# Kernel optimization log

Hardware: AMD Instinct MI355X
Metric: run time of the kernel (lower is better)

## Reference

```python
import jax, jax.numpy as jnp
import numpy as np

NUM_NODES = 100000
NUM_EDGES = 1600000
EMBED_DIM = 128
NUM_CLASSES = 2
NUM_LAYERS = 3


def setup_inputs() -> dict:
    key = jax.random.key(0)
    k_row, k_col, k_val, k_emb, k_a, k_w, k_b = jax.random.split(key, 7)
    node_indices = jnp.arange(NUM_NODES, dtype=jnp.int64 if jax.config.read('jax_enable_x64') else jnp.int32)
    adj_row = jax.random.randint(k_row, (NUM_EDGES,), 0, NUM_NODES)
    adj_col = jax.random.randint(k_col, (NUM_EDGES,), 0, NUM_NODES)
    # symmetric-normalized-ish positive edge weights
    adj_val = jax.random.uniform(k_val, (NUM_EDGES,), dtype=jnp.float32) * (1.0 / 16.0)
    embedding = jax.random.normal(k_emb, (NUM_NODES, EMBED_DIM), dtype=jnp.float32)
    alpha = jnp.ones((NUM_LAYERS + 1,), dtype=jnp.float32) / (NUM_LAYERS + 1)
    W = jax.random.normal(k_w, (EMBED_DIM, NUM_CLASSES), dtype=jnp.float32) * 0.05
    b = jnp.zeros((NUM_CLASSES,), dtype=jnp.float32)
    return {
        'node_indices': node_indices, 'adj_row': adj_row, 'adj_col': adj_col,
        'adj_val': adj_val, 'embedding': embedding, 'alpha': alpha, 'W': W, 'b': b,
    }


def reference(node_indices, adj_row, adj_col, adj_val, embedding, alpha, W, b):
    # x: [N, D] embedding lookup
    x = embedding[node_indices]
    a = jax.nn.softmax(alpha)
    # alpha-weighted running sum over propagation layers (dropout in eval mode = identity)
    acc = a[0] * x
    cur = x
    for i in range(NUM_LAYERS):
        # sparse SpMM: out[r] += val * cur[c] for each edge (r, c)
        msgs = adj_val[:, None] * cur[adj_col]          # [E, D]
        cur = jax.ops.segment_sum(msgs, adj_row, num_segments=NUM_NODES)
        acc = acc + a[i + 1] * cur
    return acc @ W + b  # [N, num_classes]
```

## Files before the change

### kernel.cpp

```cpp
#include <hip/hip_runtime.h>

#define GD(x,y) (((x)+(y)-1)/(y))

#define SH   10
#define BPR  (1 << SH)
#define G1   256
#define BS   256
#define KSPL 8

__global__ void histb_k(const int* __restrict__ row, int* __restrict__ cnt,
                        int E, int NBK, int chunk){
    __shared__ int h[128];
    for (int i = threadIdx.x; i < NBK; i += BS) h[i] = 0;
    __syncthreads();
    int s = blockIdx.x * chunk, e = min(E, s + chunk);
    for (int i = s + threadIdx.x; i < e; i += BS)
        atomicAdd(&h[row[i] >> SH], 1);
    __syncthreads();
    for (int i = threadIdx.x; i < NBK; i += BS)
        cnt[(size_t)i * G1 + blockIdx.x] = h[i];
}

__global__ void scanA_k(const int* __restrict__ in, int* __restrict__ bsum, int M){
    __shared__ int lds[256];
    int t = threadIdx.x;
    int base = blockIdx.x * 1024 + t * 4;
    int s = 0;
    #pragma unroll
    for (int j = 0; j < 4; ++j) if (base + j < M) s += in[base + j];
    lds[t] = s; __syncthreads();
    for (int off = 128; off; off >>= 1){
        if (t < off) lds[t] += lds[t + off];
        __syncthreads();
    }
    if (t == 0) bsum[blockIdx.x] = lds[0];
}

__global__ void scanB_k(int* __restrict__ bsum, int NB,
                        const float* __restrict__ alpha, float* __restrict__ a, int na){
    __shared__ int lds[1024];
    int t = threadIdx.x;
    if (t == 0){
        float m = alpha[0];
        for (int i = 1; i < na; ++i) m = fmaxf(m, alpha[i]);
        float s = 0.f;
        for (int i = 0; i < na; ++i){ float e = expf(alpha[i] - m); a[i] = e; s += e; }
        float inv = 1.f / s;
        for (int i = 0; i < na; ++i) a[i] *= inv;
    }
    int v = (t < NB) ? bsum[t] : 0;
    lds[t] = v; __syncthreads();
    for (int off = 1; off < 1024; off <<= 1){
        int add = (t >= off) ? lds[t - off] : 0;
        __syncthreads();
        lds[t] += add;
        __syncthreads();
    }
    if (t < NB) bsum[t] = lds[t] - v;
}

__global__ void scanC_k(const int* __restrict__ in, const int* __restrict__ bsum,
                        int* __restrict__ outx, int M){
    __shared__ int lds[256];
    int t = threadIdx.x;
    int base = blockIdx.x * 1024 + t * 4;
    int d[4]; int s = 0;
    #pragma unroll
    for (int j = 0; j < 4; ++j){ d[j] = (base + j < M) ? in[base + j] : 0; s += d[j]; }
    lds[t] = s; __syncthreads();
    for (int off = 1; off < 256; off <<= 1){
        int add = (t >= off) ? lds[t - off] : 0;
        __syncthreads();
        lds[t] += add;
        __syncthreads();
    }
    int run = bsum[blockIdx.x] + lds[t] - s;
    #pragma unroll
    for (int j = 0; j < 4; ++j){
        int i = base + j;
        if (i < M){ outx[i] = run; run += d[j]; }
    }
}

__global__ void fill1_k(const int* __restrict__ row, const int* __restrict__ col,
                        const float* __restrict__ val, const int* __restrict__ base,
                        int2* __restrict__ sep, int E, int NBK, int chunk){
    __shared__ int cur[128];
    for (int i = threadIdx.x; i < NBK; i += BS)
        cur[i] = base[(size_t)i * G1 + blockIdx.x];
    __syncthreads();
    int s = blockIdx.x * chunk, e = min(E, s + chunk);
    for (int i = s + threadIdx.x; i < e; i += BS){
        int r = row[i];
        int b = r >> SH;
        int pos = atomicAdd(&cur[b], 1);
        int2 pk;
        pk.x = col[i] | ((r & (BPR - 1)) << 17);
        pk.y = __float_as_int(val[i]);
        sep[pos] = pk;
    }
}

__global__ void proj_k(const float* __restrict__ emb, const int* __restrict__ idx,
                       const float* __restrict__ W, const float* __restrict__ b,
                       const float* __restrict__ a, float* __restrict__ y,
                       float* __restrict__ out, int N){
    int t = blockIdx.x * blockDim.x + threadIdx.x;
    int w = t >> 6;
    int lane = t & 63;
    int n = w * 2 + (lane >> 5);
    if (n >= N) return;
    int sl = lane & 31;
    float4 x = ((const float4*)(emb + (size_t)idx[n] * 128))[sl];
    int d0 = 4 * sl;
    float s0 = x.x * W[d0*2]   + x.y * W[d0*2+2] + x.z * W[d0*2+4] + x.w * W[d0*2+6];
    float s1 = x.x * W[d0*2+1] + x.y * W[d0*2+3] + x.z * W[d0*2+5] + x.w * W[d0*2+7];
    #pragma unroll
    for (int off = 16; off; off >>= 1){
        s0 += __shfl_down(s0, off, 32);
        s1 += __shfl_down(s1, off, 32);
    }
    if (sl == 0){
        float c = a[0];
        ((float2*)y)[n]   = make_float2(s0, s1);
        ((float2*)out)[n] = make_float2(b[0] + c * s0, b[1] + c * s1);
    }
}

__global__ void spmm_k(const int* __restrict__ bas, const int2* __restrict__ sep,
                       const float* __restrict__ yin, float* __restrict__ partial,
                       int NBK, int E){
    __shared__ float accx[BPR];
    __shared__ float accy[BPR];
    int b  = blockIdx.x / KSPL;
    int sp = blockIdx.x % KSPL;
    int t  = threadIdx.x;
    for (int j = t; j < BPR; j += BS){ accx[j] = 0.f; accy[j] = 0.f; }
    __syncthreads();
    int s = bas[(size_t)b * G1];
    int e = (b + 1 < NBK) ? bas[(size_t)(b + 1) * G1] : E;
    int len = e - s, per = GD(len, KSPL);
    int cs = s + sp * per, ce = min(e, cs + per);
    int i = cs + t;
    for (; i + 3 * BS < ce; i += 4 * BS){
        int2 p0 = sep[i], p1 = sep[i + BS], p2 = sep[i + 2*BS], p3 = sep[i + 3*BS];
        float2 m0 = ((const float2*)yin)[p0.x & 0x1FFFF];
        float2 m1 = ((const float2*)yin)[p1.x & 0x1FFFF];
        float2 m2 = ((const float2*)yin)[p2.x & 0x1FFFF];
        float2 m3 = ((const float2*)yin)[p3.x & 0x1FFFF];
        float v0 = __int_as_float(p0.y), v1 = __int_as_float(p1.y);
        float v2 = __int_as_float(p2.y), v3 = __int_as_float(p3.y);
        atomicAdd(&accx[p0.x >> 17], v0 * m0.x); atomicAdd(&accy[p0.x >> 17], v0 * m0.y);
        atomicAdd(&accx[p1.x >> 17], v1 * m1.x); atomicAdd(&accy[p1.x >> 17], v1 * m1.y);
        atomicAdd(&accx[p2.x >> 17], v2 * m2.x); atomicAdd(&accy[p2.x >> 17], v2 * m2.y);
        atomicAdd(&accx[p3.x >> 17], v3 * m3.x); atomicAdd(&accy[p3.x >> 17], v3 * m3.y);
    }
    for (; i < ce; i += BS){
        int2 pk = sep[i];
        float v = __int_as_float(pk.y);
        float2 m = ((const float2*)yin)[pk.x & 0x1FFFF];
        atomicAdd(&accx[pk.x >> 17], v * m.x);
        atomicAdd(&accy[pk.x >> 17], v * m.y);
    }
    __syncthreads();
    float2* dst = (float2*)partial + (size_t)(b * KSPL + sp) * BPR;
    for (int j = t; j < BPR; j += BS)
        dst[j] = make_float2(accx[j], accy[j]);
}

__global__ void comb_k(const float* __restrict__ partial, const float* __restrict__ a,
                       int ai, float* __restrict__ ynext, float* __restrict__ out,
                       int N, int store){
    int n = blockIdx.x * blockDim.x + threadIdx.x;
    if (n >= N) return;
    int b = n >> SH, j = n & (BPR - 1);
    const float2* p = (const float2*)partial + (size_t)b * KSPL * BPR + j;
    float sx = 0.f, sy = 0.f;
    #pragma unroll
    for (int sp = 0; sp < KSPL; ++sp){
        float2 v = p[(size_t)sp * BPR];
        sx += v.x; sy += v.y;
    }
    if (store) ((float2*)ynext)[n] = make_float2(sx, sy);
    float c = a[ai];
    float2 o = ((float2*)out)[n];
    o.x += c * sx; o.y += c * sy;
    ((float2*)out)[n] = o;
}

extern "C" void kernel_launch(void* const* d_in, const int* in_sizes, int n_in,
                              void* d_out, int out_size, void* d_ws, size_t ws_size,
                              hipStream_t stream) {
    const int*   node_idx = (const int*)  d_in[0];
    const int*   adj_row  = (const int*)  d_in[1];
    const int*   adj_col  = (const int*)  d_in[2];
    const float* adj_val  = (const float*)d_in[3];
    const float* emb      = (const float*)d_in[4];
    const float* alpha    = (const float*)d_in[5];
    const float* W        = (const float*)d_in[6];
    const float* b        = (const float*)d_in[7];
    float* out = (float*)d_out;

    const int N = in_sizes[0];
    const int E = in_sizes[1];
    const int L = in_sizes[5] - 1;
    const int NBK = GD(N, BPR);
    const int M = NBK * G1;
    const int NBA = GD(M, 1024);
    const int chunk = GD(E, G1);

    char* w = (char*)d_ws;
    float* yA     = (float*)w;  w += (size_t)N * 2 * 4;
    float* yB     = (float*)w;  w += (size_t)N * 2 * 4;
    float* partial= (float*)w;  w += (size_t)NBK * KSPL * BPR * 2 * 4;
    int2*  sep    = (int2*)w;   w += (size_t)E * 8;
    int*   cnt    = (int*)w;    w += (size_t)M * 4;
    int*   bas    = (int*)w;    w += (size_t)M * 4;
    int*   bsum   = (int*)w;    w += 4096;
    float* a      = (float*)w;

    histb_k<<<G1, BS, 0, stream>>>(adj_row, cnt, E, NBK, chunk);
    scanA_k<<<NBA, 256, 0, stream>>>(cnt, bsum, M);
    scanB_k<<<1, 1024, 0, stream>>>(bsum, NBA, alpha, a, L + 1);
    scanC_k<<<NBA, 256, 0, stream>>>(cnt, bsum, bas, M);
    fill1_k<<<G1, BS, 0, stream>>>(adj_row, adj_col, adj_val, bas, sep, E, NBK, chunk);

    proj_k<<<GD(N * 32, 256), 256, 0, stream>>>(emb, node_idx, W, b, a, yA, out, N);

    float* ysrc = yA;
    float* ydst = yB;
    for (int i = 0; i < L; ++i){
        spmm_k<<<NBK * KSPL, BS, 0, stream>>>(bas, sep, ysrc, partial, NBK, E);
        comb_k<<<GD(N, 256), 256, 0, stream>>>(partial, a, i + 1, ydst, out,
                                               N, (i < L - 1) ? 1 : 0);
        float* tmp = ysrc; ysrc = ydst; ydst = tmp;
    }
}
```

Baseline: 138.1 us.

## Replace histogram+scan bucketing with fixed-capacity buckets and atomic cursors

Removes the separate histogram kernel and the three-kernel prefix scan. Each edge bucket now gets a fixed-capacity slot (32768 entries), and a block reserves a contiguous range with one global atomic per bucket after counting locally. It also raises the split factor from 8 to 24 and uses nontemporal stores and loads for the partial sums. The cost is a larger workspace and a silent overflow if any bucket receives more than CAP edges. Edge order inside a bucket becomes nondeterministic, so float accumulation order can vary between runs.

```diff
diff --git a/kernel.cpp b/kernel.cpp
--- a/kernel.cpp
+++ b/kernel.cpp
@@ -2,44 +2,26 @@
 
 #define GD(x,y) (((x)+(y)-1)/(y))
 
-#define SH   10
-#define BPR  (1 << SH)
-#define G1   256
-#define BS   256
-#define KSPL 8
+#define SH    10
+#define BPR   (1 << SH)
+#define G1    256
+#define BS    256
+#define KSPL  24
+#define CAPSH 15
+#define CAP   (1 << CAPSH)
 
-__global__ void histb_k(const int* __restrict__ row, int* __restrict__ cnt,
-                        int E, int NBK, int chunk){
-    __shared__ int h[128];
-    for (int i = threadIdx.x; i < NBK; i += BS) h[i] = 0;
-    __syncthreads();
-    int s = blockIdx.x * chunk, e = min(E, s + chunk);
-    for (int i = s + threadIdx.x; i < e; i += BS)
-        atomicAdd(&h[row[i] >> SH], 1);
-    __syncthreads();
-    for (int i = threadIdx.x; i < NBK; i += BS)
-        cnt[(size_t)i * G1 + blockIdx.x] = h[i];
+static __device__ __forceinline__ float2 ntload2(const float2* p){
+    unsigned long long u = __builtin_nontemporal_load((const unsigned long long*)p);
+    return *(float2*)&u;
+}
+static __device__ __forceinline__ void ntstore2(float2* p, float2 v){
+    __builtin_nontemporal_store(*(unsigned long long*)&v, (unsigned long long*)p);
 }
 
-__global__ void scanA_k(const int* __restrict__ in, int* __restrict__ bsum, int M){
-    __shared__ int lds[256];
+__global__ void init_k(int* __restrict__ cursor, int NBK,
+                       const float* __restrict__ alpha, float* __restrict__ a, int na){
     int t = threadIdx.x;
-    int base = blockIdx.x * 1024 + t * 4;
-    int s = 0;
-    #pragma unroll
-    for (int j = 0; j < 4; ++j) if (base + j < M) s += in[base + j];
-    lds[t] = s; __syncthreads();
-    for (int off = 128; off; off >>= 1){
-        if (t < off) lds[t] += lds[t + off];
-        __syncthreads();
-    }
-    if (t == 0) bsum[blockIdx.x] = lds[0];
-}
-
-__global__ void scanB_k(int* __restrict__ bsum, int NB,
-                        const float* __restrict__ alpha, float* __restrict__ a, int na){
-    __shared__ int lds[1024];
-    int t = threadIdx.x;
+    if (t < NBK) cursor[t] = t << CAPSH;
     if (t == 0){
         float m = alpha[0];
         for (int i = 1; i < na; ++i) m = fmaxf(m, alpha[i]);
@@ -48,52 +30,26 @@
         float inv = 1.f / s;
         for (int i = 0; i < na; ++i) a[i] *= inv;
     }
-    int v = (t < NB) ? bsum[t] : 0;
-    lds[t] = v; __syncthreads();
-    for (int off = 1; off < 1024; off <<= 1){
-        int add = (t >= off) ? lds[t - off] : 0;
-        __syncthreads();
-        lds[t] += add;
-        __syncthreads();
-    }
-    if (t < NB) bsum[t] = lds[t] - v;
 }
 
-__global__ void scanC_k(const int* __restrict__ in, const int* __restrict__ bsum,
-                        int* __restrict__ outx, int M){
-    __shared__ int lds[256];
+__global__ void fillf_k(const int* __restrict__ row, const int* __restrict__ col,
+                        const float* __restrict__ val, int* __restrict__ cursor,
+                        int2* __restrict__ sep, int E, int NBK, int chunk){
+    __shared__ int h[128];
+    __shared__ int curb[128];
     int t = threadIdx.x;
-    int base = blockIdx.x * 1024 + t * 4;
-    int d[4]; int s = 0;
-    #pragma unroll
-    for (int j = 0; j < 4; ++j){ d[j] = (base + j < M) ? in[base + j] : 0; s += d[j]; }
-    lds[t] = s; __syncthreads();
-    for (int off = 1; off < 256; off <<= 1){
-        int add = (t >= off) ? lds[t - off] : 0;
-        __syncthreads();
-        lds[t] += add;
-        __syncthreads();
-    }
-    int run = bsum[blockIdx.x] + lds[t] - s;
-    #pragma unroll
-    for (int j = 0; j < 4; ++j){
-        int i = base + j;
-        if (i < M){ outx[i] = run; run += d[j]; }
-    }
-}
-
-__global__ void fill1_k(const int* __restrict__ row, const int* __restrict__ col,
-                        const float* __restrict__ val, const int* __restrict__ base,
-                        int2* __restrict__ sep, int E, int NBK, int chunk){
-    __shared__ int cur[128];
-    for (int i = threadIdx.x; i < NBK; i += BS)
-        cur[i] = base[(size_t)i * G1 + blockIdx.x];
+    for (int i = t; i < NBK; i += BS) h[i] = 0;
     __syncthreads();
     int s = blockIdx.x * chunk, e = min(E, s + chunk);
-    for (int i = s + threadIdx.x; i < e; i += BS){
+    for (int i = s + t; i < e; i += BS)
+        atomicAdd(&h[row[i] >> SH], 1);
+    __syncthreads();
+    if (t < NBK) curb[t] = (h[t] > 0) ? atomicAdd(&cursor[t], h[t]) : 0;
+    __syncthreads();
+    for (int i = s + t; i < e; i += BS){
         int r = row[i];
         int b = r >> SH;
-        int pos = atomicAdd(&cur[b], 1);
+        int pos = atomicAdd(&curb[b], 1);
         int2 pk;
         pk.x = col[i] | ((r & (BPR - 1)) << 17);
         pk.y = __float_as_int(val[i]);
@@ -127,9 +83,9 @@
     }
 }
 
-__global__ void spmm_k(const int* __restrict__ bas, const int2* __restrict__ sep,
+__global__ void spmm_k(const int* __restrict__ cursor, const int2* __restrict__ sep,
                        const float* __restrict__ yin, float* __restrict__ partial,
-                       int NBK, int E){
+                       int NBK){
     __shared__ float accx[BPR];
     __shared__ float accy[BPR];
     int b  = blockIdx.x / KSPL;
@@ -137,8 +93,8 @@
     int t  = threadIdx.x;
     for (int j = t; j < BPR; j += BS){ accx[j] = 0.f; accy[j] = 0.f; }
     __syncthreads();
-    int s = bas[(size_t)b * G1];
-    int e = (b + 1 < NBK) ? bas[(size_t)(b + 1) * G1] : E;
+    int s = b << CAPSH;
+    int e = cursor[b];
     int len = e - s, per = GD(len, KSPL);
     int cs = s + sp * per, ce = min(e, cs + per);
     int i = cs + t;
@@ -165,7 +121,7 @@
     __syncthreads();
     float2* dst = (float2*)partial + (size_t)(b * KSPL + sp) * BPR;
     for (int j = t; j < BPR; j += BS)
-        dst[j] = make_float2(accx[j], accy[j]);
+        ntstore2(&dst[j], make_float2(accx[j], accy[j]));
 }
 
 __global__ void comb_k(const float* __restrict__ partial, const float* __restrict__ a,
@@ -178,7 +134,7 @@
     float sx = 0.f, sy = 0.f;
     #pragma unroll
     for (int sp = 0; sp < KSPL; ++sp){
-        float2 v = p[(size_t)sp * BPR];
+        float2 v = ntload2(&p[(size_t)sp * BPR]);
         sx += v.x; sy += v.y;
     }
     if (store) ((float2*)ynext)[n] = make_float2(sx, sy);
@@ -205,32 +161,25 @@
     const int E = in_sizes[1];
     const int L = in_sizes[5] - 1;
     const int NBK = GD(N, BPR);
-    const int M = NBK * G1;
-    const int NBA = GD(M, 1024);
     const int chunk = GD(E, G1);
 
     char* w = (char*)d_ws;
     float* yA     = (float*)w;  w += (size_t)N * 2 * 4;
     float* yB     = (float*)w;  w += (size_t)N * 2 * 4;
     float* partial= (float*)w;  w += (size_t)NBK * KSPL * BPR * 2 * 4;
-    int2*  sep    = (int2*)w;   w += (size_t)E * 8;
-    int*   cnt    = (int*)w;    w += (size_t)M * 4;
-    int*   bas    = (int*)w;    w += (size_t)M * 4;
-    int*   bsum   = (int*)w;    w += 4096;
+    int2*  sep    = (int2*)w;   w += (size_t)NBK * CAP * 8;
+    int*   cursor = (int*)w;    w += 1024;
     float* a      = (float*)w;
 
-    histb_k<<<G1, BS, 0, stream>>>(adj_row, cnt, E, NBK, chunk);
-    scanA_k<<<NBA, 256, 0, stream>>>(cnt, bsum, M);
-    scanB_k<<<1, 1024, 0, stream>>>(bsum, NBA, alpha, a, L + 1);
-    scanC_k<<<NBA, 256, 0, stream>>>(cnt, bsum, bas, M);
-    fill1_k<<<G1, BS, 0, stream>>>(adj_row, adj_col, adj_val, bas, sep, E, NBK, chunk);
+    init_k<<<1, 128, 0, stream>>>(cursor, NBK, alpha, a, L + 1);
+    fillf_k<<<G1, BS, 0, stream>>>(adj_row, adj_col, adj_val, cursor, sep, E, NBK, chunk);
 
     proj_k<<<GD(N * 32, 256), 256, 0, stream>>>(emb, node_idx, W, b, a, yA, out, N);
 
     float* ysrc = yA;
     float* ydst = yB;
     for (int i = 0; i < L; ++i){
-        spmm_k<<<NBK * KSPL, BS, 0, stream>>>(bas, sep, ysrc, partial, NBK, E);
+        spmm_k<<<NBK * KSPL, BS, 0, stream>>>(cursor, sep, ysrc, partial, NBK);
         comb_k<<<GD(N, 256), 256, 0, stream>>>(partial, a, i + 1, ydst, out,
                                                N, (i < L - 1) ? 1 : 0);
         float* tmp = ysrc; ysrc = ydst; ydst = tmp;
```

Measured after the change: 128.6 us. 6.9% less time.
